# Kernel optimization log

Hardware: AMD Instinct MI355X
Metric: run time of the kernel (lower is better)

## Reference

```python
import jax, jax.numpy as jnp
import numpy as np
import math

NQ, NK, QDIM, MDIM, VDIM = 8192, 8192, 512, 512, 512
NEG = -float(1 << 32)


def setup_inputs() -> dict:
    key = jax.random.key(0)
    ks = jax.random.split(key, 8)
    Q = jax.random.normal(ks[0], (NQ, QDIM), dtype=jnp.float32)
    K = jax.random.normal(ks[1], (NK, QDIM), dtype=jnp.float32)
    V = jax.random.normal(ks[2], (NK, VDIM), dtype=jnp.float32)
    mask = jax.random.randint(ks[3], (NQ, NK), 0, 2) == 1
    s = 1.0 / math.sqrt(QDIM)
    WQ_w = jax.random.uniform(ks[4], (MDIM, QDIM), minval=-s, maxval=s, dtype=jnp.float32)
    WQ_b = jax.random.uniform(ks[5], (MDIM,), minval=-s, maxval=s, dtype=jnp.float32)
    WK_w = jax.random.uniform(ks[6], (MDIM, QDIM), minval=-s, maxval=s, dtype=jnp.float32)
    WK_b = jax.random.uniform(ks[7], (MDIM,), minval=-s, maxval=s, dtype=jnp.float32)
    return {"Q": Q, "K": K, "V": V, "WQ_w": WQ_w, "WQ_b": WQ_b,
            "WK_w": WK_w, "WK_b": WK_b, "mask": mask}


def reference(Q, K, V, WQ_w, WQ_b, WK_w, WK_b, mask):
    # Linear projections: y = x @ W^T + b
    Qp = Q @ WQ_w.T + WQ_b          # [NQ, MDIM]
    Kp = K @ WK_w.T + WK_b          # [NK, MDIM]
    scale = 1.0 / math.sqrt(MDIM)
    attn = (Qp @ Kp.T) * scale      # [NQ, NK]
    attn = jnp.where(mask, NEG, attn)
    attn = jax.nn.softmax(attn, axis=-1)
    return attn @ V                 # [NQ, VDIM]
```

## Files before the change

kernel.cpp:

```cpp
#include <hip/hip_runtime.h>

typedef __attribute__((ext_vector_type(8))) short short8;
typedef __attribute__((ext_vector_type(4))) float f32x4;

#define DEVFN __device__ __forceinline__

constexpr float SCALE_ATTN = 0.04419417382415922f;
constexpr float NEGF = -4294967296.0f;

DEVFN unsigned short f2bf(float f) {
  unsigned int u = __float_as_uint(f);
  u += 0x7FFFu + ((u >> 16) & 1u);
  return (unsigned short)(u >> 16);
}
DEVFN float bf2f(unsigned short h) { return __uint_as_float((unsigned)h << 16); }

DEVFN void gl_lds16(const void* g, void* l) {
  __builtin_amdgcn_global_load_lds(
      (const __attribute__((address_space(1))) unsigned int*)g,
      (__attribute__((address_space(3))) unsigned int*)l, 16, 0, 0);
}

DEVFN float dpp_fmax16(float x) {
  int v;
  v = __builtin_amdgcn_update_dpp(0, __float_as_int(x), 0xB1, 0xF, 0xF, true);
  x = fmaxf(x, __int_as_float(v));
  v = __builtin_amdgcn_update_dpp(0, __float_as_int(x), 0x4E, 0xF, 0xF, true);
  x = fmaxf(x, __int_as_float(v));
  v = __builtin_amdgcn_update_dpp(0, __float_as_int(x), 0x141, 0xF, 0xF, true);
  x = fmaxf(x, __int_as_float(v));
  v = __builtin_amdgcn_update_dpp(0, __float_as_int(x), 0x140, 0xF, 0xF, true);
  x = fmaxf(x, __int_as_float(v));
  return x;
}
DEVFN float dpp_fadd16(float x) {
  int v;
  v = __builtin_amdgcn_update_dpp(0, __float_as_int(x), 0xB1, 0xF, 0xF, true);
  x += __int_as_float(v);
  v = __builtin_amdgcn_update_dpp(0, __float_as_int(x), 0x4E, 0xF, 0xF, true);
  x += __int_as_float(v);
  v = __builtin_amdgcn_update_dpp(0, __float_as_int(x), 0x141, 0xF, 0xF, true);
  x += __int_as_float(v);
  v = __builtin_amdgcn_update_dpp(0, __float_as_int(x), 0x140, 0xF, 0xF, true);
  x += __int_as_float(v);
  return x;
}

__global__ void k_detect(const unsigned int* __restrict__ q, const unsigned int* __restrict__ m,
                         int* __restrict__ fflag, int* __restrict__ esize) {
  int lane = threadIdx.x;
  if (blockIdx.x == 0) {
    unsigned bad = 0;
    for (int i = 0; i < 64; i++) {
      unsigned v = q[i * 64 + lane];
      unsigned h = v & 0xFFFFu;
      unsigned e = (h >> 7) & 0xFFu;
      if (h != 0u && (e < 96u || e > 150u)) bad = 1;
    }
    unsigned long long anyb = __ballot(bad != 0);
    if (lane == 0) *fflag = (anyb == 0ULL) ? 1 : 0;
  } else {
    unsigned okd = 1, okh = 1, okb = 1;
    for (int i = 0; i < 64; i++) {
      unsigned v = m[i * 64 + lane];
      if (v > 1u && v != 0x3F800000u) okd = 0;
      unsigned h0 = v & 0xFFFFu, h1 = v >> 16;
      if ((h0 && h0 != 0x3F80u && h0 != 1u) || (h1 && h1 != 0x3F80u && h1 != 1u)) okh = 0;
      if (v & 0xFEFEFEFEu) okb = 0;
    }
    okd = (__ballot(okd == 0) == 0ULL);
    okh = (__ballot(okh == 0) == 0ULL);
    okb = (__ballot(okb == 0) == 0ULL);
    if (lane == 0) *esize = okd ? 4 : (okh ? 2 : 1);
  }
}

__global__ void k_prep(const void* __restrict__ Q, unsigned short* __restrict__ Qb,
                       const void* __restrict__ K, unsigned short* __restrict__ Kb,
                       const void* __restrict__ Wq, unsigned short* __restrict__ Wqb,
                       const void* __restrict__ Wk, unsigned short* __restrict__ Wkb,
                       const void* __restrict__ bq, unsigned short* __restrict__ bqb,
                       const void* __restrict__ bk, unsigned short* __restrict__ bkb,
                       const int* __restrict__ bf16flag) {
  int blk = blockIdx.x;
  const void* src; unsigned short* dst; int base, n;
  if (blk < 2048)      { src = Q;  dst = Qb;  base = blk;        n = 8192 * 512; }
  else if (blk < 4096) { src = K;  dst = Kb;  base = blk - 2048; n = 8192 * 512; }
  else if (blk < 4224) { src = Wq; dst = Wqb; base = blk - 4096; n = 512 * 512; }
  else if (blk < 4352) { src = Wk; dst = Wkb; base = blk - 4224; n = 512 * 512; }
  else if (blk == 4352){ src = bq; dst = bqb; base = 0;          n = 512; }
  else                 { src = bk; dst = bkb; base = 0;          n = 512; }
  int i = (base * 256 + threadIdx.x) * 8;
  if (i >= n) return;
  if (*bf16flag) {
    *(uint4*)(dst + i) = *(const uint4*)((const unsigned short*)src + i);
  } else {
    const float* f = (const float*)src + i;
    float4 a = *(const float4*)f, b = *(const float4*)(f + 4);
    uint4 o;
    o.x = (unsigned)f2bf(a.x) | ((unsigned)f2bf(a.y) << 16);
    o.y = (unsigned)f2bf(a.z) | ((unsigned)f2bf(a.w) << 16);
    o.z = (unsigned)f2bf(b.x) | ((unsigned)f2bf(b.y) << 16);
    o.w = (unsigned)f2bf(b.z) | ((unsigned)f2bf(b.w) << 16);
    *(uint4*)(dst + i) = o;
  }
}

__global__ void k_transpose_v(const void* __restrict__ Vsrc, const int* __restrict__ bf16flag,
                              unsigned short* __restrict__ Vt) {
  __shared__ unsigned short T[64][72];
  int t = threadIdx.x;
  int rb = blockIdx.x, cb = blockIdx.y;
  int r = t >> 3, c8 = (t & 7) * 8;
  int isbf = *bf16flag;
#pragma unroll
  for (int j = 0; j < 2; j++) {
    int row = rb * 64 + j * 32 + r;
    unsigned short e[8];
    if (isbf) {
      alignas(16) unsigned short tmp[8];
      *(uint4*)tmp = *(const uint4*)((const unsigned short*)Vsrc + (size_t)row * 512 + cb * 64 + c8);
#pragma unroll
      for (int i = 0; i < 8; i++) e[i] = tmp[i];
    } else {
      const float* f = (const float*)Vsrc + (size_t)row * 512 + cb * 64 + c8;
      float4 a = *(const float4*)f, b = *(const float4*)(f + 4);
      e[0] = f2bf(a.x); e[1] = f2bf(a.y); e[2] = f2bf(a.z); e[3] = f2bf(a.w);
      e[4] = f2bf(b.x); e[5] = f2bf(b.y); e[6] = f2bf(b.z); e[7] = f2bf(b.w);
    }
#pragma unroll
    for (int i = 0; i < 8; i++) T[c8 + i][j * 32 + r] = e[i];
  }
  __syncthreads();
#pragma unroll
  for (int j = 0; j < 2; j++) {
    int d = cb * 64 + j * 32 + r;
    alignas(16) unsigned short o[8];
#pragma unroll
    for (int i = 0; i < 8; i++) o[i] = T[j * 32 + r][c8 + i];
    int tt = rb * 2 + (c8 >> 5);
    *(uint4*)(Vt + ((size_t)tt * 512 + d) * 32 + (c8 & 31)) = *(const uint4*)o;
  }
}

DEVFN unsigned nib4(unsigned v) {
  unsigned t = v; t |= t >> 1; t |= t >> 2; t |= t >> 4; t &= 0x01010101u;
  return (t * 0x10204080u) >> 28;
}
DEVFN unsigned pair2(unsigned v) {
  unsigned t = v; t |= t >> 8; t |= t >> 4; t |= t >> 2; t |= t >> 1;
  return (t & 1u) | (((t >> 16) & 1u) << 1);
}
__global__ void k_pack(const void* __restrict__ mask, const int* __restrict__ esize,
                       unsigned long long* __restrict__ bits) {
  int wv = (blockIdx.x * blockDim.x + threadIdx.x) >> 6;
  int lane = threadIdx.x & 63;
  int sz = *esize;
  if (sz == 4) {
    const unsigned int* m = (const unsigned int*)mask;
    for (int g = wv; g < 262144; g += 4096) {
      size_t base = (size_t)g * 256 + lane;
      unsigned v0 = m[base], v1 = m[base + 64], v2 = m[base + 128], v3 = m[base + 192];
      unsigned long long b0 = __ballot(v0 != 0u);
      unsigned long long b1 = __ballot(v1 != 0u);
      unsigned long long b2 = __ballot(v2 != 0u);
      unsigned long long b3 = __ballot(v3 != 0u);
      if (lane == 0) {
        bits[g * 4 + 0] = b0; bits[g * 4 + 1] = b1;
        bits[g * 4 + 2] = b2; bits[g * 4 + 3] = b3;
      }
    }
  } else if (sz == 2) {
    const uint4* m = (const uint4*)mask;
    for (int g = wv; g < 131072; g += 4096) {
      uint4 v = m[(size_t)g * 64 + lane];
      unsigned c8 = pair2(v.x) | (pair2(v.y) << 2) | (pair2(v.z) << 4) | (pair2(v.w) << 6);
      unsigned long long x = (unsigned long long)c8 << ((lane & 7) * 8);
      x |= __shfl_xor(x, 1); x |= __shfl_xor(x, 2); x |= __shfl_xor(x, 4);
      if ((lane & 7) == 0) bits[g * 8 + (lane >> 3)] = x;
    }
  } else {
    const uint4* m = (const uint4*)mask;
    for (int g = wv; g < 65536; g += 4096) {
      uint4 v = m[(size_t)g * 64 + lane];
      unsigned c16 = nib4(v.x) | (nib4(v.y) << 4) | (nib4(v.z) << 8) | (nib4(v.w) << 12);
      unsigned long long x = (unsigned long long)c16 << ((lane & 3) * 16);
      x |= __shfl_xor(x, 1); x |= __shfl_xor(x, 2);
      if ((lane & 3) == 0) bits[g * 16 + (lane >> 2)] = x;
    }
  }
}

__global__ __launch_bounds__(256, 2) void k_proj(
    const unsigned short* __restrict__ Aq, const unsigned short* __restrict__ Wq,
    const unsigned short* __restrict__ bq, unsigned short* __restrict__ outq,
    const unsigned short* __restrict__ Ak, const unsigned short* __restrict__ Wk,
    const unsigned short* __restrict__ bk, unsigned short* __restrict__ outk) {
  const unsigned short* A = blockIdx.z ? Ak : Aq;
  const unsigned short* W = blockIdx.z ? Wk : Wq;
  const unsigned short* bias = blockIdx.z ? bk : bq;
  unsigned short* out = blockIdx.z ? outk : outq;

  __shared__ alignas(16) unsigned short As[128 * 64];
  __shared__ alignas(16) unsigned short Bs[128 * 64];
  int tid = threadIdx.x, lane = tid & 63, wave = tid >> 6;
  int wi = wave >> 1, wj = wave & 1;
  int l15 = lane & 15, l4 = lane >> 4;
  int rowbase = blockIdx.x * 128, colbase = blockIdx.y * 128;
  f32x4 acc[4][4];
#pragma unroll
  for (int i = 0; i < 4; i++)
#pragma unroll
    for (int j = 0; j < 4; j++) acc[i][j] = f32x4{0.f, 0.f, 0.f, 0.f};

  int swr = l15 & 7;
  for (int kb = 0; kb < 512; kb += 64) {
    __syncthreads();
#pragma unroll
    for (int t = 0; t < 4; t++) {
      int inst = wave * 4 + t;
      int r = inst * 8 + (lane >> 3);
      int c = ((lane & 7) ^ (r & 7)) * 8;
      gl_lds16(A + (size_t)(rowbase + r) * 512 + kb + c, &As[inst * 512]);
      gl_lds16(W + (size_t)(colbase + r) * 512 + kb + c, &Bs[inst * 512]);
    }
    __syncthreads();
#pragma unroll
    for (int t2 = 0; t2 < 2; t2++) {
      short8 a[4], b[4];
#pragma unroll
      for (int i = 0; i < 4; i++) {
        int row = wi * 64 + i * 16 + l15;
        a[i] = *(const short8*)&As[row * 64 + (((t2 * 4 + l4) ^ swr) * 8)];
      }
#pragma unroll
      for (int j = 0; j < 4; j++) {
        int row = wj * 64 + j * 16 + l15;
        b[j] = *(const short8*)&Bs[row * 64 + (((t2 * 4 + l4) ^ swr) * 8)];
      }
#pragma unroll
      for (int i = 0; i < 4; i++)
#pragma unroll
        for (int j = 0; j < 4; j++)
          acc[i][j] = __builtin_amdgcn_mfma_f32_16x16x32_bf16(a[i], b[j], acc[i][j], 0, 0, 0);
    }
  }
#pragma unroll
  for (int j = 0; j < 4; j++) {
    int col = colbase + wj * 64 + j * 16 + l15;
    float bj = bf2f(bias[col]);
#pragma unroll
    for (int i = 0; i < 4; i++) {
      int row0 = rowbase + wi * 64 + i * 16 + l4 * 4;
#pragma unroll
      for (int r = 0; r < 4; r++)
        out[(size_t)(row0 + r) * 512 + col] = f2bf(acc[i][j][r] + bj);
    }
  }
}

__global__ __launch_bounds__(512, 2) void k_attn(
    const unsigned short* __restrict__ Qp, const unsigned short* __restrict__ Kp,
    const unsigned short* __restrict__ Vt, const unsigned long long* __restrict__ mbits,
    unsigned short* __restrict__ Opart, float* __restrict__ mpart, float* __restrict__ lpart) {
  __shared__ alignas(16) unsigned short KB[16384];
  __shared__ alignas(16) unsigned short VB[16384];
  __shared__ alignas(16) unsigned short P2[4][128][8];
  __shared__ alignas(16) float alds[128];
  __shared__ alignas(16) int nfl[8];
  int tid = threadIdx.x, lane = tid & 63, wave = tid >> 6;
  int l15 = lane & 15, l4 = lane >> 4;
  int b = blockIdx.x;
  int split = b & 7;
  int qb = (b >> 3) * 128;

  short8 qf[16];
  {
    int row = qb + wave * 16 + l15;
#pragma unroll
    for (int t = 0; t < 16; t++)
      qf[t] = *(const short8*)(Qp + (size_t)row * 512 + t * 32 + l4 * 8);
  }
  f32x4 o[8][4];
#pragma unroll
  for (int i = 0; i < 8; i++)
#pragma unroll
    for (int j = 0; j < 4; j++) o[i][j] = f32x4{0.f, 0.f, 0.f, 0.f};
  float mi[4] = {NEGF, NEGF, NEGF, NEGF};
  float li[4] = {0.f, 0.f, 0.f, 0.f};

  int swK = l15 | ((l15 & 3) << 4);
  const unsigned int* mb32 = (const unsigned int*)mbits;

  {
    int tv = split * 32;
#pragma unroll
    for (int t = 0; t < 4; t++) {
      int r = wave * 4 + t;
      int swz = (r & 15) | ((r & 3) << 4);
      gl_lds16(Kp + (size_t)(tv * 32 + r) * 512 + ((lane ^ swz) * 8), &KB[r * 512]);
    }
  }

  for (int it = 0; it < 32; it++) {
    int tv = split * 32 + it;

    __syncthreads();

#pragma unroll
    for (int t = 0; t < 4; t++) {
      int inst = wave * 4 + t;
      int d = inst * 16 + (lane >> 2);
      int cg = (lane & 3) ^ ((d >> 2) & 3);
      gl_lds16(Vt + (size_t)tv * 16384 + d * 32 + cg * 8, &VB[inst * 512]);
    }

    unsigned mw[4];
#pragma unroll
    for (int r = 0; r < 4; r++)
      mw[r] = mb32[((size_t)(qb + wave * 16 + l4 * 4 + r) * 128 + split * 16 + (it >> 1)) * 2 + (it & 1)];

    f32x4 sacc[2];
#pragma unroll
    for (int c = 0; c < 2; c++) sacc[c] = f32x4{0.f, 0.f, 0.f, 0.f};
#pragma unroll
    for (int t2 = 0; t2 < 16; t2++) {
      short8 a = qf[t2];
#pragma unroll
      for (int c = 0; c < 2; c++) {
        int row = c * 16 + l15;
        short8 bb = *(const short8*)&KB[row * 512 + (((t2 * 4 + l4) ^ swK) * 8)];
        sacc[c] = __builtin_amdgcn_mfma_f32_16x16x32_bf16(a, bb, sacc[c], 0, 0, 0);
      }
    }

#pragma unroll
    for (int c = 0; c < 2; c++)
#pragma unroll
      for (int r = 0; r < 4; r++) {
        float s = sacc[c][r] * SCALE_ATTN;
        bool msk = (mw[r] >> (c * 16 + l15)) & 1u;
        sacc[c][r] = msk ? NEGF : s;
      }

    float al4[4];
    bool need = false;
#pragma unroll
    for (int r = 0; r < 4; r++) {
      float t = dpp_fmax16(fmaxf(sacc[0][r], sacc[1][r]));
      al4[r] = t;
      need |= (t > mi[r] + 8.0f);
    }
    unsigned long long blt = __ballot(need);
    if (lane == 0) nfl[wave] = (blt != 0ULL) ? 1 : 0;
    if (blt) {
#pragma unroll
      for (int r = 0; r < 4; r++) {
        float mn = fmaxf(mi[r], al4[r]);
        float a = __expf(mi[r] - mn);
        li[r] *= a;
        mi[r] = mn;
        al4[r] = a;
      }
    } else {
#pragma unroll
      for (int r = 0; r < 4; r++) al4[r] = 1.0f;
    }
    if (l15 == 0) *(f32x4*)&alds[wave * 16 + l4 * 4] = f32x4{al4[0], al4[1], al4[2], al4[3]};

#pragma unroll
    for (int c = 0; c < 2; c++)
#pragma unroll
      for (int r = 0; r < 4; r++) sacc[c][r] = __expf(sacc[c][r] - mi[r]);
#pragma unroll
    for (int r = 0; r < 4; r++)
      li[r] += dpp_fadd16(sacc[0][r] + sacc[1][r]);

#pragma unroll
    for (int r = 0; r < 4; r++) {
      int prow = wave * 16 + l4 * 4 + r;
#pragma unroll
      for (int c = 0; c < 2; c++)
        P2[c * 2 + (l15 >> 3)][prow][l15 & 7] = f2bf(sacc[c][r]);
    }

    __syncthreads();

    {
      int tv1 = (it < 31) ? tv + 1 : tv;
#pragma unroll
      for (int t = 0; t < 4; t++) {
        int r = wave * 4 + t;
        int swz = (r & 15) | ((r & 3) << 4);
        gl_lds16(Kp + (size_t)(tv1 * 32 + r) * 512 + ((lane ^ swz) * 8), &KB[r * 512]);
      }
    }

    {
      const int4* n4 = (const int4*)nfl;
      int4 na = n4[0], nb4 = n4[1];
      if (na.x | na.y | na.z | na.w | nb4.x | nb4.y | nb4.z | nb4.w) {
#pragma unroll
        for (int rf = 0; rf < 8; rf++) {
          f32x4 av = *(const f32x4*)&alds[rf * 16 + l4 * 4];
#pragma unroll
          for (int df = 0; df < 4; df++)
#pragma unroll
            for (int j = 0; j < 4; j++) o[rf][df][j] *= av[j];
        }
      }
    }

    short8 vf[4];
#pragma unroll
    for (int df = 0; df < 4; df++) {
      int d = wave * 64 + df * 16 + l15;
      vf[df] = *(const short8*)&VB[d * 32 + ((l4 ^ ((l15 >> 2) & 3)) * 8)];
    }
#pragma unroll
    for (int rf = 0; rf < 8; rf++) {
      short8 pa = *(const short8*)&P2[l4][rf * 16 + l15][0];
#pragma unroll
      for (int df = 0; df < 4; df++)
        o[rf][df] = __builtin_amdgcn_mfma_f32_16x16x32_bf16(pa, vf[df], o[rf][df], 0, 0, 0);
    }
  }

#pragma unroll
  for (int r = 0; r < 4; r++) {
    int row = qb + wave * 16 + l4 * 4 + r;
    if (l15 == 0) {
      mpart[(size_t)split * 8192 + row] = mi[r];
      lpart[(size_t)split * 8192 + row] = li[r];
    }
  }
  uint2* op2 = (uint2*)Opart;
#pragma unroll
  for (int rf = 0; rf < 8; rf++)
#pragma unroll
    for (int df = 0; df < 4; df++) {
      int f = wave * 4 + df;
      uint2 v;
      v.x = (unsigned)f2bf(o[rf][df][0]) | ((unsigned)f2bf(o[rf][df][1]) << 16);
      v.y = (unsigned)f2bf(o[rf][df][2]) | ((unsigned)f2bf(o[rf][df][3]) << 16);
      op2[(((size_t)b * 32 + f) * 8 + rf) * 64 + l4 * 16 + l15] = v;
    }
}

__global__ void k_combine(const unsigned short* __restrict__ Opart,
                          const float* __restrict__ mpart, const float* __restrict__ lpart,
                          float* __restrict__ out) {
  int q = blockIdx.x;
  int half = blockIdx.y;
  int tid = threadIdx.x;
  int wave = tid >> 6, lane = tid & 63, l4 = (lane >> 4) & 3, l15 = lane & 15;
  int row0 = q * 128 + wave * 16 + l4 * 4;

  float w[8][4], inv[4];
#pragma unroll
  for (int r = 0; r < 4; r++) {
    float M = NEGF;
    float mv[8];
#pragma unroll
    for (int s = 0; s < 8; s++) { mv[s] = mpart[s * 8192 + row0 + r]; M = fmaxf(M, mv[s]); }
    float L = 0.f;
#pragma unroll
    for (int s = 0; s < 8; s++) {
      float ws = __expf(mv[s] - M);
      w[s][r] = ws;
      L += ws * lpart[s * 8192 + row0 + r];
    }
    inv[r] = 1.0f / L;
  }
  const uint2* op2 = (const uint2*)Opart;
#pragma unroll
  for (int fo = 0; fo < 16; fo++) {
    int f = half * 16 + fo;
    float acc[4] = {0.f, 0.f, 0.f, 0.f};
#pragma unroll
    for (int s = 0; s < 8; s++) {
      uint2 v = op2[(((size_t)(q * 8 + s) * 32 + f) * 8 + wave) * 64 + l4 * 16 + l15];
      acc[0] += w[s][0] * bf2f((unsigned short)(v.x & 0xFFFFu));
      acc[1] += w[s][1] * bf2f((unsigned short)(v.x >> 16));
      acc[2] += w[s][2] * bf2f((unsigned short)(v.y & 0xFFFFu));
      acc[3] += w[s][3] * bf2f((unsigned short)(v.y >> 16));
    }
    int col = f * 16 + l15;
#pragma unroll
    for (int r = 0; r < 4; r++)
      out[(size_t)(row0 + r) * 512 + col] = acc[r] * inv[r];
  }
}

extern "C" void kernel_launch(void* const* d_in, const int* in_sizes, int n_in,
                              void* d_out, int out_size, void* d_ws, size_t ws_size,
                              hipStream_t stream) {
  const void* Q   = d_in[0];
  const void* K   = d_in[1];
  const void* V   = d_in[2];
  const void* WQw = d_in[3];
  const void* WQb = d_in[4];
  const void* WKw = d_in[5];
  const void* WKb = d_in[6];
  const void* mask = d_in[7];
  float* out = (float*)d_out;
  char* ws = (char*)d_ws;
  (void)in_sizes; (void)n_in; (void)out_size; (void)ws_size;

  constexpr size_t SZ_MAT = (size_t)8192 * 512 * 2;
  size_t off = 4096;
  unsigned short* Qb  = (unsigned short*)(ws + off); off += SZ_MAT;
  unsigned short* Kb  = (unsigned short*)(ws + off); off += SZ_MAT;
  unsigned short* Wqb = (unsigned short*)(ws + off); off += (size_t)512 * 512 * 2;
  unsigned short* Wkb = (unsigned short*)(ws + off); off += (size_t)512 * 512 * 2;
  unsigned short* bqb = (unsigned short*)(ws + off); off += 1024;
  unsigned short* bkb = (unsigned short*)(ws + off); off += 1024;
  unsigned short* Vt  = (unsigned short*)(ws + off); off += SZ_MAT;
  unsigned short* Qp  = (unsigned short*)(ws + off); off += SZ_MAT;
  unsigned short* Kp  = (unsigned short*)(ws + off); off += SZ_MAT;
  unsigned long long* mbits = (unsigned long long*)(ws + off); off += (size_t)8192 * 128 * 8;
  unsigned short* Opart = (unsigned short*)(ws + off); off += (size_t)512 * 512 * 32 * 8;
  float* mpart = (float*)(ws + off); off += (size_t)8 * 8192 * 4;
  float* lpart = (float*)(ws + off); off += (size_t)8 * 8192 * 4;
  int* fflag = (int*)ws;
  int* esize = (int*)(ws + 64);

  k_detect<<<2, 64, 0, stream>>>((const unsigned int*)Q, (const unsigned int*)mask, fflag, esize);
  k_prep<<<4354, 256, 0, stream>>>(Q, Qb, K, Kb, WQw, Wqb, WKw, Wkb, WQb, bqb, WKb, bkb, fflag);
  k_transpose_v<<<dim3(128, 8), 256, 0, stream>>>(V, fflag, Vt);
  k_pack<<<1024, 256, 0, stream>>>(mask, esize, mbits);
  k_proj<<<dim3(64, 4, 2), 256, 0, stream>>>(Qb, Wqb, bqb, Qp, Kb, Wkb, bkb, Kp);
  k_attn<<<512, 512, 0, stream>>>(Qp, Kp, Vt, mbits, Opart, mpart, lpart);
  k_combine<<<dim3(64, 2), 512, 0, stream>>>(Opart, mpart, lpart, out);
}
```

Measured before the change: 823.1 us.

## Software-pipeline attention loop: double-buffer K and P, overlap PV with next QK

Double-buffers the K tile, the P tile, the rescale factors and the rescale flags in LDS. Each iteration now runs the previous tile's P·V MFMAs before the current tile's QK^T MFMAs and softmax, and the final P·V is drained after the loop. This cuts the loop from two __syncthreads to one manual waitcnt plus barrier, and the K prefetch for the next tile is issued at the top of the iteration. MFMA sections are also wrapped in s_setprio. The larger LDS footprint, about 112KB, likely leaves room for only one 512-thread block per CU instead of the two requested by launch bounds, which may reduce latency hiding.

```diff
diff --git a/kernel.cpp b/kernel.cpp
--- a/kernel.cpp
+++ b/kernel.cpp
@@ -263,11 +263,11 @@
     const unsigned short* __restrict__ Qp, const unsigned short* __restrict__ Kp,
     const unsigned short* __restrict__ Vt, const unsigned long long* __restrict__ mbits,
     unsigned short* __restrict__ Opart, float* __restrict__ mpart, float* __restrict__ lpart) {
-  __shared__ alignas(16) unsigned short KB[16384];
+  __shared__ alignas(16) unsigned short KB[2][16384];
   __shared__ alignas(16) unsigned short VB[16384];
-  __shared__ alignas(16) unsigned short P2[4][128][8];
-  __shared__ alignas(16) float alds[128];
-  __shared__ alignas(16) int nfl[8];
+  __shared__ alignas(16) unsigned short P2[2][4][128][8];
+  __shared__ alignas(16) float alds[2][128];
+  __shared__ alignas(16) int nfl[2][8];
   int tid = threadIdx.x, lane = tid & 63, wave = tid >> 6;
   int l15 = lane & 15, l4 = lane >> 4;
   int b = blockIdx.x;
@@ -298,14 +298,65 @@
     for (int t = 0; t < 4; t++) {
       int r = wave * 4 + t;
       int swz = (r & 15) | ((r & 3) << 4);
-      gl_lds16(Kp + (size_t)(tv * 32 + r) * 512 + ((lane ^ swz) * 8), &KB[r * 512]);
-    }
-  }
+      gl_lds16(Kp + (size_t)(tv * 32 + r) * 512 + ((lane ^ swz) * 8), &KB[0][r * 512]);
+    }
+  }
+  __builtin_amdgcn_s_waitcnt(0x0F70);
+  __builtin_amdgcn_s_barrier();
 
   for (int it = 0; it < 32; it++) {
+    int cur = it & 1, prv = cur ^ 1;
     int tv = split * 32 + it;
 
-    __syncthreads();
+    unsigned mw[4];
+#pragma unroll
+    for (int r = 0; r < 4; r++)
+      mw[r] = mb32[((size_t)(qb + wave * 16 + l4 * 4 + r) * 128 + split * 16 + (it >> 1)) * 2 + (it & 1)];
+    asm volatile("" ::: "memory");
+
+    {
+      int tv1 = (it < 31) ? tv + 1 : tv;
+#pragma unroll
+      for (int t = 0; t < 4; t++) {
+        int r = wave * 4 + t;
+        int swz = (r & 15) | ((r & 3) << 4);
+        gl_lds16(Kp + (size_t)(tv1 * 32 + r) * 512 + ((lane ^ swz) * 8), &KB[prv][r * 512]);
+      }
+    }
+
+    if (it) {
+      __builtin_amdgcn_s_waitcnt(0x0F78);
+      __builtin_amdgcn_sched_barrier(0);
+      {
+        const int4* n4 = (const int4*)&nfl[prv][0];
+        int4 na = n4[0], nb4 = n4[1];
+        if (na.x | na.y | na.z | na.w | nb4.x | nb4.y | nb4.z | nb4.w) {
+#pragma unroll
+          for (int rf = 0; rf < 8; rf++) {
+            f32x4 av = *(const f32x4*)&alds[prv][rf * 16 + l4 * 4];
+#pragma unroll
+            for (int df = 0; df < 4; df++)
+#pragma unroll
+              for (int j = 0; j < 4; j++) o[rf][df][j] *= av[j];
+          }
+        }
+      }
+      short8 vf[4];
+#pragma unroll
+      for (int df = 0; df < 4; df++) {
+        int d = wave * 64 + df * 16 + l15;
+        vf[df] = *(const short8*)&VB[d * 32 + ((l4 ^ ((l15 >> 2) & 3)) * 8)];
+      }
+      __builtin_amdgcn_s_setprio(1);
+#pragma unroll
+      for (int rf = 0; rf < 8; rf++) {
+        short8 pa = *(const short8*)&P2[prv][l4][rf * 16 + l15][0];
+#pragma unroll
+        for (int df = 0; df < 4; df++)
+          o[rf][df] = __builtin_amdgcn_mfma_f32_16x16x32_bf16(pa, vf[df], o[rf][df], 0, 0, 0);
+      }
+      __builtin_amdgcn_s_setprio(0);
+    }
 
 #pragma unroll
     for (int t = 0; t < 4; t++) {
@@ -315,24 +366,21 @@
       gl_lds16(Vt + (size_t)tv * 16384 + d * 32 + cg * 8, &VB[inst * 512]);
     }
 
-    unsigned mw[4];
-#pragma unroll
-    for (int r = 0; r < 4; r++)
-      mw[r] = mb32[((size_t)(qb + wave * 16 + l4 * 4 + r) * 128 + split * 16 + (it >> 1)) * 2 + (it & 1)];
-
     f32x4 sacc[2];
 #pragma unroll
     for (int c = 0; c < 2; c++) sacc[c] = f32x4{0.f, 0.f, 0.f, 0.f};
+    __builtin_amdgcn_s_setprio(1);
 #pragma unroll
     for (int t2 = 0; t2 < 16; t2++) {
       short8 a = qf[t2];
 #pragma unroll
       for (int c = 0; c < 2; c++) {
         int row = c * 16 + l15;
-        short8 bb = *(const short8*)&KB[row * 512 + (((t2 * 4 + l4) ^ swK) * 8)];
+        short8 bb = *(const short8*)&KB[cur][row * 512 + (((t2 * 4 + l4) ^ swK) * 8)];
         sacc[c] = __builtin_amdgcn_mfma_f32_16x16x32_bf16(a, bb, sacc[c], 0, 0, 0);
       }
     }
+    __builtin_amdgcn_s_setprio(0);
 
 #pragma unroll
     for (int c = 0; c < 2; c++)
@@ -352,7 +400,7 @@
       need |= (t > mi[r] + 8.0f);
     }
     unsigned long long blt = __ballot(need);
-    if (lane == 0) nfl[wave] = (blt != 0ULL) ? 1 : 0;
+    if (lane == 0) nfl[cur][wave] = (blt != 0ULL) ? 1 : 0;
     if (blt) {
 #pragma unroll
       for (int r = 0; r < 4; r++) {
@@ -366,7 +414,7 @@
 #pragma unroll
       for (int r = 0; r < 4; r++) al4[r] = 1.0f;
     }
-    if (l15 == 0) *(f32x4*)&alds[wave * 16 + l4 * 4] = f32x4{al4[0], al4[1], al4[2], al4[3]};
+    if (l15 == 0) *(f32x4*)&alds[cur][wave * 16 + l4 * 4] = f32x4{al4[0], al4[1], al4[2], al4[3]};
 
 #pragma unroll
     for (int c = 0; c < 2; c++)
@@ -381,36 +429,28 @@
       int prow = wave * 16 + l4 * 4 + r;
 #pragma unroll
       for (int c = 0; c < 2; c++)
-        P2[c * 2 + (l15 >> 3)][prow][l15 & 7] = f2bf(sacc[c][r]);
-    }
-
-    __syncthreads();
-
-    {
-      int tv1 = (it < 31) ? tv + 1 : tv;
-#pragma unroll
-      for (int t = 0; t < 4; t++) {
-        int r = wave * 4 + t;
-        int swz = (r & 15) | ((r & 3) << 4);
-        gl_lds16(Kp + (size_t)(tv1 * 32 + r) * 512 + ((lane ^ swz) * 8), &KB[r * 512]);
-      }
-    }
-
-    {
-      const int4* n4 = (const int4*)nfl;
-      int4 na = n4[0], nb4 = n4[1];
-      if (na.x | na.y | na.z | na.w | nb4.x | nb4.y | nb4.z | nb4.w) {
-#pragma unroll
-        for (int rf = 0; rf < 8; rf++) {
-          f32x4 av = *(const f32x4*)&alds[rf * 16 + l4 * 4];
-#pragma unroll
-          for (int df = 0; df < 4; df++)
-#pragma unroll
-            for (int j = 0; j < 4; j++) o[rf][df][j] *= av[j];
-        }
-      }
-    }
-
+        P2[cur][c * 2 + (l15 >> 3)][prow][l15 & 7] = f2bf(sacc[c][r]);
+    }
+
+    __builtin_amdgcn_s_waitcnt(0x0074);
+    __builtin_amdgcn_s_barrier();
+  }
+
+  __builtin_amdgcn_s_waitcnt(0x0F70);
+  __builtin_amdgcn_sched_barrier(0);
+  {
+    const int4* n4 = (const int4*)&nfl[1][0];
+    int4 na = n4[0], nb4 = n4[1];
+    if (na.x | na.y | na.z | na.w | nb4.x | nb4.y | nb4.z | nb4.w) {
+#pragma unroll
+      for (int rf = 0; rf < 8; rf++) {
+        f32x4 av = *(const f32x4*)&alds[1][rf * 16 + l4 * 4];
+#pragma unroll
+        for (int df = 0; df < 4; df++)
+#pragma unroll
+          for (int j = 0; j < 4; j++) o[rf][df][j] *= av[j];
+      }
+    }
     short8 vf[4];
 #pragma unroll
     for (int df = 0; df < 4; df++) {
@@ -419,7 +459,7 @@
     }
 #pragma unroll
     for (int rf = 0; rf < 8; rf++) {
-      short8 pa = *(const short8*)&P2[l4][rf * 16 + l15][0];
+      short8 pa = *(const short8*)&P2[1][l4][rf * 16 + l15][0];
 #pragma unroll
       for (int df = 0; df < 4; df++)
         o[rf][df] = __builtin_amdgcn_mfma_f32_16x16x32_bf16(pa, vf[df], o[rf][df], 0, 0, 0);
```

After: 791.7 us. -3.8%, faster.
